# Optimization experiments

Measured on AMD Instinct MI355X. Metric: run time of the kernel, lower is better.

## Reference

```python
import jax, jax.numpy as jnp
import numpy as np

H_IMG = 256; W_IMG = 256; C = 256
WIN = (16, 16); STRIPE = (32, 32); DF = 4; NH = 4
ASZ = (STRIPE[0] // DF, STRIPE[1] // DF)
TS = ((STRIPE[0] + ASZ[0]) // 2, (STRIPE[1] + ASZ[1]) // 2)  # stripe bias table half-size (20,20)


def _win_part(x, ws):
    # (B,H,W,c) -> (B*nW, ws0*ws1, c)
    B, H, W, c = x.shape
    x = x.reshape(B, H // ws[0], ws[0], W // ws[1], ws[1], c)
    return x.transpose(0, 1, 3, 2, 4, 5).reshape(-1, ws[0] * ws[1], c)


def _win_rev(w, ws, H, W):
    c = w.shape[-1]
    B = w.shape[0] // ((H // ws[0]) * (W // ws[1]))
    x = w.reshape(B, H // ws[0], W // ws[1], ws[0], ws[1], c)
    return x.transpose(0, 1, 3, 2, 4, 5).reshape(B, H, W, c)


def _l2n(x):
    # F.normalize(dim=-1)
    return x / jnp.maximum(jnp.linalg.norm(x, axis=-1, keepdims=True), 1e-12)


def _affine(attn, logit_scale, w1, b1, w2, table, index):
    # attn: (B_, nH, N1, N2); AffineTransform with mask=None
    N1, N2 = attn.shape[-2], attn.shape[-1]
    attn = attn * jnp.exp(jnp.minimum(logit_scale, np.log(100.0)))  # clamp max=log(1/0.01)
    bt = jax.nn.relu(table.reshape(-1, 2) @ w1 + b1) @ w2  # (T, nH)
    bias = bt[index.reshape(-1)].reshape(N1, N2, -1).transpose(2, 0, 1)  # (nH,N1,N2)
    return attn + (16.0 * jax.nn.sigmoid(bias))[None]


def _coords(start, size):
    h = np.arange(start[0], start[0] + size[0])
    w = np.arange(start[1], start[1] + size[1])
    return np.stack(np.meshgrid(h, w, indexing='ij')).reshape(2, -1)


def _idx(c1, c2, md):
    d = (c1[:, :, None] - c2[:, None, :]).transpose(1, 2, 0).astype(np.int64)
    return (d[..., 0] + md[0] - 1) * (2 * md[1] - 1) + (d[..., 1] + md[1] - 1)


def _table(ts):
    h = np.arange(-(ts[0] - 1), ts[0], dtype=np.float32) / (ts[0] - 1)
    w = np.arange(-(ts[1] - 1), ts[1], dtype=np.float32) / (ts[1] - 1)
    t = np.stack(np.meshgrid(h, w, indexing='ij'), axis=-1)[None] * 8.0
    return (np.sign(t) * np.log2(np.abs(t) + 1.0) / np.log2(8.0)).astype(np.float32)


def setup_inputs():
    ks = iter(jax.random.split(jax.random.key(0), 32))
    def nrm(shape, s=0.02):
        return jax.random.normal(next(ks), shape, dtype=jnp.float32) * s
    inp = {}
    inp['x'] = jax.random.normal(next(ks), (1, H_IMG * W_IMG, C), dtype=jnp.float32)
    inp['qkv_w'] = nrm((C, 3 * C)); inp['qkv_b'] = nrm((3 * C,))
    inp['anchor_w'] = nrm((C, C // 2)); inp['anchor_b'] = nrm((C // 2,))
    for tag in ['w', 's1', 's2']:
        inp['ls_' + tag] = jnp.full((NH, 1, 1), np.log(10.0), dtype=jnp.float32)
        inp['cpb_w1_' + tag] = nrm((2, 512), 0.1)
        inp['cpb_b1_' + tag] = nrm((512,), 0.1)
        inp['cpb_w2_' + tag] = nrm((512, NH), 0.1)
    inp['proj_w'] = nrm((C, C)); inp['proj_b'] = nrm((C,))
    inp['table_w'] = jnp.asarray(_table(WIN))
    inp['table_s'] = jnp.asarray(_table(TS))
    cw = _coords((0, 0), WIN)
    inp['index_w'] = jnp.asarray(_idx(cw, cw, WIN), dtype=jnp.int32)
    cs = _coords((0, 0), STRIPE)
    st = ((STRIPE[0] - ASZ[0]) // 2, (STRIPE[1] - ASZ[1]) // 2)
    ca = _coords(st, ASZ)
    inp['index_a2w'] = jnp.asarray(_idx(ca, cs, TS), dtype=jnp.int32)
    inp['index_w2a'] = jnp.asarray(_idx(cs, ca, TS), dtype=jnp.int32)
    return inp


def reference(x, qkv_w, qkv_b, anchor_w, anchor_b,
              ls_w, cpb_w1_w, cpb_b1_w, cpb_w2_w,
              ls_s1, cpb_w1_s1, cpb_b1_s1, cpb_w2_s1,
              ls_s2, cpb_w1_s2, cpb_b1_s2, cpb_w2_s2,
              proj_w, proj_b, table_w, table_s,
              index_w, index_a2w, index_w2a):
    B, L, c = x.shape
    qkv = x @ qkv_w + qkv_b               # (B, L, 3C)
    half = 3 * c // 2
    hd = half // 3 // NH                  # head_dim per branch
    # ---- window attention on first half of qkv channels ----
    qw = _win_part(qkv[..., :half].reshape(B, H_IMG, W_IMG, half), WIN)  # (B_, N, 3*C/2)
    B_, N, _ = qw.shape
    q, k, v = qw.reshape(B_, N, 3, NH, hd).transpose(2, 0, 3, 1, 4)
    attn = jnp.einsum('bhnd,bhmd->bhnm', _l2n(q), _l2n(k))
    attn = jax.nn.softmax(_affine(attn, ls_w, cpb_w1_w, cpb_b1_w, cpb_w2_w, table_w, index_w), axis=-1)
    xw = jnp.einsum('bhnm,bhmd->bhnd', attn, v).transpose(0, 2, 1, 3).reshape(B_, N, NH * hd)
    xw = _win_rev(xw, WIN, H_IMG, W_IMG).reshape(B, L, c // 2)
    # ---- anchor projection: AvgPool2d(DF) + Linear(C -> C/2) ----
    xi = x.reshape(B, H_IMG, W_IMG, c)
    pooled = xi.reshape(B, H_IMG // DF, DF, W_IMG // DF, DF, c).mean(axis=(2, 4))
    anchor = pooled @ anchor_w + anchor_b  # (B, H/DF, W/DF, C/2)
    # ---- anchor stripe attention on second half ----
    qs = _win_part(qkv[..., half:].reshape(B, H_IMG, W_IMG, half), STRIPE)  # (Bs, N1, 3*C/2)
    Bs, N1, _ = qs.shape
    anc = _win_part(anchor, ASZ)           # (Bs, N2, C/2)
    N2 = anc.shape[1]
    q, k, v = qs.reshape(Bs, N1, 3, NH, hd).transpose(2, 0, 3, 1, 4)
    anc = anc.reshape(Bs, N2, NH, hd).transpose(0, 2, 1, 3)
    a1 = jnp.einsum('bhnd,bhmd->bhnm', _l2n(anc), _l2n(k))   # (Bs,NH,N2,N1)
    a1 = jax.nn.softmax(_affine(a1, ls_s1, cpb_w1_s1, cpb_b1_s1, cpb_w2_s1, table_s, index_a2w), axis=-1)
    xm = jnp.einsum('bhnm,bhmd->bhnd', a1, v)                # (Bs,NH,N2,hd)
    a2 = jnp.einsum('bhnd,bhmd->bhnm', _l2n(q), _l2n(anc))   # (Bs,NH,N1,N2)
    a2 = jax.nn.softmax(_affine(a2, ls_s2, cpb_w1_s2, cpb_b1_s2, cpb_w2_s2, table_s, index_w2a), axis=-1)
    xs = jnp.einsum('bhnm,bhmd->bhnd', a2, xm).transpose(0, 2, 1, 3).reshape(Bs, N1, NH * hd)
    xs = _win_rev(xs, STRIPE, H_IMG, W_IMG).reshape(B, L, c // 2)
    # ---- merge + output projection ----
    return jnp.concatenate([xw, xs], axis=-1) @ proj_w + proj_b
```

## Files before the change

### kernel.cpp

```cpp
#include <hip/hip_runtime.h>
#include <cstdint>
#include <cstddef>

typedef unsigned short u16;
typedef __attribute__((ext_vector_type(8))) short short8;
typedef __attribute__((ext_vector_type(4))) float floatx4;
typedef __attribute__((ext_vector_type(4))) unsigned int uintx4;
typedef __attribute__((ext_vector_type(2))) unsigned int uintx2;

__device__ __forceinline__ float bf2f(u16 u){
  union { unsigned int i; float f; } v; v.i = ((unsigned int)u) << 16; return v.f;
}
__device__ __forceinline__ u16 f2bf(float f){
  union { float ff; unsigned int i; } v; v.ff = f;
  return (u16)((v.i + 0x7fffu + ((v.i >> 16) & 1u)) >> 16);
}
__device__ __forceinline__ unsigned int pk2(float a, float b){
  return (unsigned int)f2bf(a) | ((unsigned int)f2bf(b) << 16);
}
__device__ __forceinline__ void load32(const u16* p, float* v){
  const uintx4* p4 = (const uintx4*)p;
#pragma unroll
  for (int c = 0; c < 4; ++c){
    uintx4 u = p4[c];
    v[c*8+0] = bf2f((u16)(u.x & 0xffffu)); v[c*8+1] = bf2f((u16)(u.x >> 16));
    v[c*8+2] = bf2f((u16)(u.y & 0xffffu)); v[c*8+3] = bf2f((u16)(u.y >> 16));
    v[c*8+4] = bf2f((u16)(u.z & 0xffffu)); v[c*8+5] = bf2f((u16)(u.z >> 16));
    v[c*8+6] = bf2f((u16)(u.w & 0xffffu)); v[c*8+7] = bf2f((u16)(u.w >> 16));
  }
}
__device__ __forceinline__ void norm_store(u16* dst, const float* v, int t, int strideU16){
  float ss = 0.f;
#pragma unroll
  for (int e = 0; e < 32; ++e) ss += v[e]*v[e];
  float inv = 1.f / fmaxf(sqrtf(ss), 1e-12f);
#pragma unroll
  for (int q = 0; q < 4; ++q){
    uintx4 u;
    u.x = pk2(v[q*8+0]*inv, v[q*8+1]*inv);
    u.y = pk2(v[q*8+2]*inv, v[q*8+3]*inv);
    u.z = pk2(v[q*8+4]*inv, v[q*8+5]*inv);
    u.w = pk2(v[q*8+6]*inv, v[q*8+7]*inv);
    *(uintx4*)(dst + q*strideU16 + t*8) = u;
  }
}
__device__ __forceinline__ float expc(float a){
  return __expf(fminf(a, 30.f));
}
__device__ __forceinline__ uintx4 ld8f_bf(const float* g){
  floatx4 u0 = *(const floatx4*)g;
  floatx4 u1 = *(const floatx4*)(g + 4);
  uintx4 w;
  w.x = pk2(u0.x, u0.y); w.y = pk2(u0.z, u0.w);
  w.z = pk2(u1.x, u1.y); w.w = pk2(u1.z, u1.w);
  return w;
}
__device__ __forceinline__ float redq(float v){
  v += __shfl_xor(v, 16); v += __shfl_xor(v, 32);
  return v;
}

__global__ void transpose_w(const float* __restrict__ qkv_w, const float* __restrict__ anchor_w,
                            const float* __restrict__ proj_w,
                            u16* __restrict__ qkvt, u16* __restrict__ anct, u16* __restrict__ projt){
  int id = blockIdx.x*256 + threadIdx.x;
  if (id < 196608){ int k = id / 768, n = id % 768; qkvt[n*256 + k] = f2bf(qkv_w[id]); }
  else if (id < 229376){ int r = id - 196608; int k = r / 128, n = r % 128; anct[n*256 + k] = f2bf(anchor_w[r]); }
  else { int r = id - 229376; int k = r >> 8, n = r & 255; projt[n*256 + k] = f2bf(proj_w[r]); }
}

__global__ void cpb_mlp(const float* __restrict__ tw, const float* __restrict__ ts,
                        const float* __restrict__ w1w, const float* __restrict__ b1w, const float* __restrict__ w2w,
                        const float* __restrict__ w1s1, const float* __restrict__ b1s1, const float* __restrict__ w2s1,
                        const float* __restrict__ w1s2, const float* __restrict__ b1s2, const float* __restrict__ w2s2,
                        float* __restrict__ btw, float* __restrict__ bts1, float* __restrict__ bts2){
  int tag = blockIdx.y;
  const float *tab, *w1, *b1, *w2; float* bt; int T;
  if (tag == 0){ tab = tw; w1 = w1w;  b1 = b1w;  w2 = w2w;  bt = btw;  T = 961; }
  else if (tag == 1){ tab = ts; w1 = w1s1; b1 = b1s1; w2 = w2s1; bt = bts1; T = 1521; }
  else { tab = ts; w1 = w1s2; b1 = b1s2; w2 = w2s2; bt = bts2; T = 1521; }
  __shared__ float sw1[2][512];
  __shared__ float sb1[512];
  __shared__ float sw2[512][4];
  for (int j = threadIdx.x; j < 512; j += 256){
    sw1[0][j] = w1[j]; sw1[1][j] = w1[512 + j]; sb1[j] = b1[j];
    for (int h = 0; h < 4; ++h) sw2[j][h] = w2[j*4 + h];
  }
  __syncthreads();
  int idx = blockIdx.x*256 + threadIdx.x;
  int r = idx >> 2, hh = idx & 3;
  if (r < T){
    float t0 = tab[2*r], t1 = tab[2*r + 1];
    float acc = 0.f;
    for (int j = 0; j < 512; ++j){
      float hj = fmaxf(fmaf(t0, sw1[0][j], fmaf(t1, sw1[1][j], sb1[j])), 0.f);
      acc = fmaf(hj, sw2[j][hh], acc);
    }
    bt[r*4 + hh] = acc;
  }
}

__global__ void bias_gather(const float* __restrict__ btw, const float* __restrict__ bts1,
                            const float* __restrict__ bts2,
                            const int* __restrict__ idxw, const int* __restrict__ idxa2w,
                            const int* __restrict__ idxw2a,
                            float* __restrict__ bw, float* __restrict__ bs1, float* __restrict__ bs2){
  int id = blockIdx.x*256 + threadIdx.x;
  int which = id >> 18;
  int rem = id & 262143;
  int h = rem >> 16, e = rem & 65535;
  const float* bt; const int* ix; float* dst;
  if (which == 0){ bt = btw;  ix = idxw;   dst = bw;  }
  else if (which == 1){ bt = bts1; ix = idxa2w; dst = bs1; }
  else { bt = bts2; ix = idxw2a; dst = bs2; }
  float v = bt[ix[e]*4 + h];
  dst[h*65536 + e] = 16.f / (1.f + expc(-v));
}

__global__ void avgpool(const float* __restrict__ x, float* __restrict__ pooled){
  int a = blockIdx.x, c = threadIdx.x;
  int ay = a >> 6, ax = a & 63;
  float acc = 0.f;
#pragma unroll
  for (int dy = 0; dy < 4; ++dy)
#pragma unroll
    for (int dx = 0; dx < 4; ++dx)
      acc += x[(size_t)((ay*4 + dy)*256 + ax*4 + dx)*256 + c];
  pooled[(size_t)a*256 + c] = acc * 0.0625f;
}

__launch_bounds__(256, 2)
__global__ void gemm_bt(const float* __restrict__ A, const u16* __restrict__ Bt,
                        const float* __restrict__ bias, u16* __restrict__ C,
                        int M, int N, int K){
  __shared__ __align__(16) u16 lsA[4096];
  __shared__ __align__(16) u16 lsB[4096];
  const int tid = threadIdx.x, lane = tid & 63, wv = tid >> 6;
  const int lane15 = lane & 15, quad = lane >> 4;
  const int wr = wv >> 1, wc = wv & 1;
  const int m0 = blockIdx.x * 128, n0 = blockIdx.y * 128;
  floatx4 acc[4][4] = {};
  for (int k0 = 0; k0 < K; k0 += 32){
    uintx4 ra[2], rb[2];
#pragma unroll
    for (int c = 0; c < 2; ++c){
      int f = c*256 + tid, row = f & 127, q = f >> 7;
      ra[c] = ld8f_bf(A + (size_t)(m0 + row)*K + k0 + q*8);
      rb[c] = *(const uintx4*)(Bt + (size_t)(n0 + row)*K + k0 + q*8);
    }
#pragma unroll
    for (int c = 0; c < 2; ++c){
      int f = c*256 + tid;
      *(uintx4*)(lsA + f*8) = ra[c];
      *(uintx4*)(lsB + f*8) = rb[c];
    }
    __syncthreads();
    short8 a[4], b[4];
#pragma unroll
    for (int i = 0; i < 4; ++i)
      a[i] = *(const short8*)(lsA + quad*1024 + (wr*64 + i*16 + lane15)*8);
#pragma unroll
    for (int j = 0; j < 4; ++j)
      b[j] = *(const short8*)(lsB + quad*1024 + (wc*64 + j*16 + lane15)*8);
#pragma unroll
    for (int i = 0; i < 4; ++i)
#pragma unroll
      for (int j = 0; j < 4; ++j)
        acc[i][j] = __builtin_amdgcn_mfma_f32_16x16x32_bf16(a[i], b[j], acc[i][j], 0, 0, 0);
    __syncthreads();
  }
#pragma unroll
  for (int j = 0; j < 4; ++j){
    int col = n0 + wc*64 + j*16 + lane15;
    float bz = bias[col];
#pragma unroll
    for (int i = 0; i < 4; ++i){
      int rowb = m0 + wr*64 + i*16 + quad*4;
#pragma unroll
      for (int r = 0; r < 4; ++r)
        C[(size_t)(rowb + r)*N + col] = f2bf(acc[i][j][r] + bz);
    }
  }
}

__launch_bounds__(256, 2)
__global__ void gemm_proj_inplace(float* __restrict__ AC, const u16* __restrict__ Bt,
                                  const float* __restrict__ bias){
  __shared__ __align__(16) u16 lsA[4096];
  __shared__ __align__(16) u16 lsB[8192];
  const int tid = threadIdx.x, lane = tid & 63, wv = tid >> 6;
  const int lane15 = lane & 15, quad = lane >> 4;
  const int wr = wv >> 1, wc = wv & 1;
  const int m0 = blockIdx.x * 128;
  floatx4 acc[4][8] = {};
  for (int k0 = 0; k0 < 256; k0 += 32){
    uintx4 ra[2], rb[4];
#pragma unroll
    for (int c = 0; c < 2; ++c){
      int f = c*256 + tid, row = f & 127, q = f >> 7;
      ra[c] = ld8f_bf(AC + (size_t)(m0 + row)*256 + k0 + q*8);
    }
#pragma unroll
    for (int c = 0; c < 4; ++c){
      int f = c*256 + tid, row = f & 255, q = f >> 8;
      rb[c] = *(const uintx4*)(Bt + (size_t)row*256 + k0 + q*8);
    }
#pragma unroll
    for (int c = 0; c < 2; ++c){ int f = c*256 + tid; *(uintx4*)(lsA + f*8) = ra[c]; }
#pragma unroll
    for (int c = 0; c < 4; ++c){ int f = c*256 + tid; *(uintx4*)(lsB + f*8) = rb[c]; }
    __syncthreads();
    short8 a[4], b[8];
#pragma unroll
    for (int i = 0; i < 4; ++i)
      a[i] = *(const short8*)(lsA + quad*1024 + (wr*64 + i*16 + lane15)*8);
#pragma unroll
    for (int j = 0; j < 8; ++j)
      b[j] = *(const short8*)(lsB + quad*2048 + (wc*128 + j*16 + lane15)*8);
#pragma unroll
    for (int i = 0; i < 4; ++i)
#pragma unroll
      for (int j = 0; j < 8; ++j)
        acc[i][j] = __builtin_amdgcn_mfma_f32_16x16x32_bf16(a[i], b[j], acc[i][j], 0, 0, 0);
    __syncthreads();
  }
#pragma unroll
  for (int j = 0; j < 8; ++j){
    int col = wc*128 + j*16 + lane15;
    float bz = bias[col];
#pragma unroll
    for (int i = 0; i < 4; ++i){
      int rowb = m0 + wr*64 + i*16 + quad*4;
#pragma unroll
      for (int r = 0; r < 4; ++r)
        AC[(size_t)(rowb + r)*256 + col] = acc[i][j][r] + bz;
    }
  }
}

__launch_bounds__(256, 3)
__global__ void win_attn(const u16* __restrict__ qkvh, const float* __restrict__ lsw,
                         const float* __restrict__ biasw, float* __restrict__ outm, int r0){
  __shared__ __align__(16) u16 sm[24576];
  const int tid = threadIdx.x, lane = tid & 63, wv = tid >> 6;
  const int lane15 = lane & 15, quad = lane >> 4;
  const int h = blockIdx.y;
  const int wyl = blockIdx.x >> 4, wx = blockIdx.x & 15;
  u16* Ks = sm;
  u16* Qs = sm + 8192;
  u16* VT = sm + 16384;
  {
    int t = tid;
    int pyl = wyl*16 + (t >> 4), px = wx*16 + (t & 15);
    const u16* base = qkvh + (size_t)(pyl*256 + px)*384 + h*32;
    float v[32];
    load32(base, v);        norm_store(Qs, v, t, 2048);
    load32(base + 128, v);  norm_store(Ks, v, t, 2048);
    load32(base + 256, v);
    int kq = t >> 3, e = t & 7;
#pragma unroll
    for (int d = 0; d < 32; ++d) VT[kq*256 + d*8 + e] = f2bf(v[d]);
  }
  __syncthreads();
  short8 qf[4];
#pragma unroll
  for (int j = 0; j < 4; ++j)
    qf[j] = *(const short8*)(Qs + quad*2048 + (wv*64 + j*16 + lane15)*8);
  __syncthreads();

  float scale = __expf(fminf(lsw[h], 4.6051702f));
  float off = fminf(scale + 16.f, 80.f);
  const float* bptr = biasw + ((size_t)h << 16);
  u16* Pw = Qs + wv*2048;
  const floatx4 zf4 = {0.f, 0.f, 0.f, 0.f};
  floatx4 accO[2][4] = {};
  float lsum[4] = {};

  for (int kc = 0; kc < 8; ++kc){
    floatx4 bia[2][4];
#pragma unroll
    for (int i = 0; i < 2; ++i)
#pragma unroll
      for (int j = 0; j < 4; ++j)
        bia[i][j] = *(const floatx4*)(bptr + (size_t)(wv*64 + j*16 + lane15)*256 + kc*32 + i*16 + quad*4);
    short8 kf[2];
#pragma unroll
    for (int i = 0; i < 2; ++i)
      kf[i] = *(const short8*)(Ks + quad*2048 + (kc*32 + i*16 + lane15)*8);
#pragma unroll
    for (int i = 0; i < 2; ++i)
#pragma unroll
      for (int j = 0; j < 4; ++j){
        floatx4 sv = __builtin_amdgcn_mfma_f32_16x16x32_bf16(kf[i], qf[j], zf4, 0, 0, 0);
        float p0 = expc(fmaf(sv[0], scale, bia[i][j][0]) - off);
        float p1 = expc(fmaf(sv[1], scale, bia[i][j][1]) - off);
        float p2 = expc(fmaf(sv[2], scale, bia[i][j][2]) - off);
        float p3 = expc(fmaf(sv[3], scale, bia[i][j][3]) - off);
        lsum[j] += (p0 + p1) + (p2 + p3);
        uintx2 w; w.x = pk2(p0, p1); w.y = pk2(p2, p3);
        *(uintx2*)(Pw + (i*2 + (quad>>1))*512 + (j*16 + lane15)*8 + (quad&1)*4) = w;
      }
    asm volatile("s_waitcnt lgkmcnt(0)" ::: "memory");
    short8 ptf[4], vtf[2];
#pragma unroll
    for (int j = 0; j < 4; ++j)
      ptf[j] = *(const short8*)(Pw + quad*512 + (j*16 + lane15)*8);
#pragma unroll
    for (int m = 0; m < 2; ++m)
      vtf[m] = *(const short8*)(VT + (kc*4 + quad)*256 + (m*16 + lane15)*8);
#pragma unroll
    for (int m = 0; m < 2; ++m)
#pragma unroll
      for (int j = 0; j < 4; ++j)
        accO[m][j] = __builtin_amdgcn_mfma_f32_16x16x32_bf16(vtf[m], ptf[j], accO[m][j], 0, 0, 0);
  }
  float linv[4];
#pragma unroll
  for (int j = 0; j < 4; ++j) linv[j] = 1.f / redq(lsum[j]);
#pragma unroll
  for (int m = 0; m < 2; ++m)
#pragma unroll
    for (int j = 0; j < 4; ++j){
      int tok = wv*64 + j*16 + lane15;
      int py = r0 + wyl*16 + (tok >> 4), px = wx*16 + (tok & 15);
      floatx4 o = accO[m][j] * linv[j];
      *(floatx4*)(outm + (size_t)(py*256 + px)*256 + h*32 + m*16 + quad*4) = o;
    }
}

__launch_bounds__(256, 3)
__global__ void stripe_xm(const u16* __restrict__ qkvh, const u16* __restrict__ anchor,
                          const float* __restrict__ ls1, const float* __restrict__ bias1,
                          float* __restrict__ gl1, u16* __restrict__ gO, int r0){
  __shared__ __align__(16) u16 sm[18432];
  const int tid = threadIdx.x, lane = tid & 63, wv = tid >> 6;
  const int lane15 = lane & 15, quad = lane >> 4;
  const int s = blockIdx.x, h = blockIdx.y, kb = blockIdx.z;
  const int syl = s >> 3, sx = s & 7;
  u16* ANC = sm; u16* KC = sm + 2048; u16* VT = sm + 6144; u16* P1T = sm + 10240;
  if (tid < 64){
    int ay = (r0 >> 2) + syl*8 + (tid >> 3), ax = sx*8 + (tid & 7);
    float v[32]; load32(anchor + (size_t)(ay*64 + ax)*128 + h*32, v);
    norm_store(ANC, v, tid, 512);
  }
  __syncthreads();
  short8 ancf = *(const short8*)(ANC + quad*512 + (wv*16 + lane15)*8);
  float scale1 = __expf(fminf(ls1[h], 4.6051702f));
  float off1 = fminf(scale1 + 16.f, 80.f);
  const float* b1p = bias1 + ((size_t)h << 16) + (size_t)(wv*16 + lane15)*1024;
  const floatx4 zf4 = {0.f, 0.f, 0.f, 0.f};
  floatx4 accO1[2] = {};
  float l1 = 0.f;
  for (int kc = 0; kc < 4; ++kc){
    int kkb = kb*512 + kc*128;
    { int t = tid;
      if (t < 128){
        int tok = kkb + t;
        int pyl = syl*32 + (tok >> 5), px = sx*32 + (tok & 31);
        float v[32]; load32(qkvh + (size_t)(pyl*256 + px)*384 + 128 + h*32, v);
        norm_store(KC, v, t, 1024);
      } else {
        int t2 = t - 128, tok = kkb + t2;
        int pyl = syl*32 + (tok >> 5), px = sx*32 + (tok & 31);
        float v[32]; load32(qkvh + (size_t)(pyl*256 + px)*384 + 256 + h*32, v);
        int kq = t2 >> 3, e = t2 & 7;
#pragma unroll
        for (int d = 0; d < 32; ++d) VT[kq*256 + d*8 + e] = f2bf(v[d]);
      }
    }
    __syncthreads();
    floatx4 bia[8];
#pragma unroll
    for (int i = 0; i < 8; ++i)
      bia[i] = *(const floatx4*)(b1p + kkb + i*16 + quad*4);
#pragma unroll
    for (int i = 0; i < 8; ++i){
      short8 kf = *(const short8*)(KC + quad*1024 + (i*16 + lane15)*8);
      floatx4 sv = __builtin_amdgcn_mfma_f32_16x16x32_bf16(kf, ancf, zf4, 0, 0, 0);
      float p0 = expc(fmaf(sv[0], scale1, bia[i][0]) - off1);
      float p1 = expc(fmaf(sv[1], scale1, bia[i][1]) - off1);
      float p2 = expc(fmaf(sv[2], scale1, bia[i][2]) - off1);
      float p3 = expc(fmaf(sv[3], scale1, bia[i][3]) - off1);
      l1 += (p0 + p1) + (p2 + p3);
      uintx2 w; w.x = pk2(p0, p1); w.y = pk2(p2, p3);
      *(uintx2*)(P1T + (i*2 + (quad>>1))*512 + (wv*16 + lane15)*8 + (quad&1)*4) = w;
    }
    asm volatile("s_waitcnt lgkmcnt(0)" ::: "memory");
#pragma unroll
    for (int ks = 0; ks < 4; ++ks){
      short8 ptf = *(const short8*)(P1T + (ks*4 + quad)*512 + (wv*16 + lane15)*8);
#pragma unroll
      for (int m = 0; m < 2; ++m){
        short8 vtf = *(const short8*)(VT + (ks*4 + quad)*256 + (m*16 + lane15)*8);
        accO1[m] = __builtin_amdgcn_mfma_f32_16x16x32_bf16(vtf, ptf, accO1[m], 0, 0, 0);
      }
    }
    __syncthreads();
  }
  l1 = redq(l1);
  int ent = (s*4 + h)*2 + kb;
  if (quad == 0) gl1[ent*64 + wv*16 + lane15] = l1;
#pragma unroll
  for (int m = 0; m < 2; ++m){
    uintx2 w; w.x = pk2(accO1[m][0], accO1[m][1]); w.y = pk2(accO1[m][2], accO1[m][3]);
    *(uintx2*)(gO + (size_t)ent*2048 + (wv*16 + lane15)*32 + m*16 + quad*4) = w;
  }
}

__launch_bounds__(256, 3)
__global__ void stripe_xs(const u16* __restrict__ qkvh, const u16* __restrict__ anchor,
                          const float* __restrict__ ls2, const float* __restrict__ bias2,
                          const float* __restrict__ gl1, const u16* __restrict__ gO,
                          float* __restrict__ outm, int r0){
  __shared__ __align__(16) u16 sm[20480];
  const int tid = threadIdx.x, lane = tid & 63, wv = tid >> 6;
  const int lane15 = lane & 15, quad = lane >> 4;
  const int s = blockIdx.x >> 2, qc = blockIdx.x & 3, h = blockIdx.y;
  const int syl = s >> 3, sx = s & 7;
  u16* ANC = sm;
  u16* XMT = sm + 2048;
  u16* QW  = sm + 4096 + wv*2048;
  u16* P2T = sm + 12288 + wv*2048;
  if (tid < 64){
    int ay = (r0 >> 2) + syl*8 + (tid >> 3), ax = sx*8 + (tid & 7);
    float v[32]; load32(anchor + (size_t)(ay*64 + ax)*128 + h*32, v);
    norm_store(ANC, v, tid, 512);
  }
  {
    int a = tid >> 2, db = (tid & 3)*8;
    int e0 = (s*4 + h)*2;
    float inv = 1.f / (gl1[e0*64 + a] + gl1[(e0 + 1)*64 + a]);
    uintx4 u0 = *(const uintx4*)(gO + (size_t)e0*2048 + a*32 + db);
    uintx4 u1 = *(const uintx4*)(gO + (size_t)(e0 + 1)*2048 + a*32 + db);
    unsigned int w0[4] = {u0.x, u0.y, u0.z, u0.w};
    unsigned int w1[4] = {u1.x, u1.y, u1.z, u1.w};
#pragma unroll
    for (int c = 0; c < 4; ++c){
      float a0 = bf2f((u16)(w0[c] & 0xffffu)) + bf2f((u16)(w1[c] & 0xffffu));
      float a1 = bf2f((u16)(w0[c] >> 16))     + bf2f((u16)(w1[c] >> 16));
      XMT[(a >> 3)*256 + (db + c*2)*8     + (a & 7)] = f2bf(a0 * inv);
      XMT[(a >> 3)*256 + (db + c*2 + 1)*8 + (a & 7)] = f2bf(a1 * inv);
    }
  }
  __syncthreads();
  int tq = qc*256 + wv*64;
  { int tok = tq + lane;
    int pyl = syl*32 + (tok >> 5), px = sx*32 + (tok & 31);
    float v[32]; load32(qkvh + (size_t)(pyl*256 + px)*384 + h*32, v);
    norm_store(QW, v, lane, 512);
  }
  asm volatile("s_waitcnt lgkmcnt(0)" ::: "memory");
  short8 qf2[4];
#pragma unroll
  for (int j = 0; j < 4; ++j)
    qf2[j] = *(const short8*)(QW + quad*512 + (j*16 + lane15)*8);
  float scale2 = __expf(fminf(ls2[h], 4.6051702f));
  float off2 = fminf(scale2 + 16.f, 80.f);
  const float* b2p = bias2 + ((size_t)h << 16);
  const floatx4 zf4 = {0.f, 0.f, 0.f, 0.f};
  floatx4 accO2[2][4] = {};
  float l2[4] = {};
#pragma unroll
  for (int c = 0; c < 2; ++c){
    floatx4 bia[2][4];
#pragma unroll
    for (int i = 0; i < 2; ++i)
#pragma unroll
      for (int j = 0; j < 4; ++j)
        bia[i][j] = *(const floatx4*)(b2p + (size_t)(tq + j*16 + lane15)*64 + c*32 + i*16 + quad*4);
    short8 af[2];
#pragma unroll
    for (int i = 0; i < 2; ++i)
      af[i] = *(const short8*)(ANC + quad*512 + (c*32 + i*16 + lane15)*8);
#pragma unroll
    for (int i = 0; i < 2; ++i)
#pragma unroll
      for (int j = 0; j < 4; ++j){
        floatx4 sv = __builtin_amdgcn_mfma_f32_16x16x32_bf16(af[i], qf2[j], zf4, 0, 0, 0);
        float p0 = expc(fmaf(sv[0], scale2, bia[i][j][0]) - off2);
        float p1 = expc(fmaf(sv[1], scale2, bia[i][j][1]) - off2);
        float p2 = expc(fmaf(sv[2], scale2, bia[i][j][2]) - off2);
        float p3 = expc(fmaf(sv[3], scale2, bia[i][j][3]) - off2);
        l2[j] += (p0 + p1) + (p2 + p3);
        uintx2 w; w.x = pk2(p0, p1); w.y = pk2(p2, p3);
        *(uintx2*)(P2T + (i*2 + (quad>>1))*512 + (j*16 + lane15)*8 + (quad&1)*4) = w;
      }
    asm volatile("s_waitcnt lgkmcnt(0)" ::: "memory");
    short8 ptf[4], xmf[2];
#pragma unroll
    for (int j = 0; j < 4; ++j)
      ptf[j] = *(const short8*)(P2T + quad*512 + (j*16 + lane15)*8);
#pragma unroll
    for (int m = 0; m < 2; ++m)
      xmf[m] = *(const short8*)(XMT + (c*4 + quad)*256 + (m*16 + lane15)*8);
#pragma unroll
    for (int m = 0; m < 2; ++m)
#pragma unroll
      for (int j = 0; j < 4; ++j)
        accO2[m][j] = __builtin_amdgcn_mfma_f32_16x16x32_bf16(xmf[m], ptf[j], accO2[m][j], 0, 0, 0);
  }
  float linv[4];
#pragma unroll
  for (int j = 0; j < 4; ++j) linv[j] = 1.f / redq(l2[j]);
#pragma unroll
  for (int m = 0; m < 2; ++m)
#pragma unroll
    for (int j = 0; j < 4; ++j){
      int tok = tq + j*16 + lane15;
      int py = r0 + syl*32 + (tok >> 5), px = sx*32 + (tok & 31);
      floatx4 o = accO2[m][j] * linv[j];
      *(floatx4*)(outm + (size_t)(py*256 + px)*256 + 128 + h*32 + m*16 + quad*4) = o;
    }
}

extern "C" void kernel_launch(void* const* d_in, const int* in_sizes, int n_in,
                              void* d_out, int out_size, void* d_ws, size_t ws_size,
                              hipStream_t stream) {
  (void)in_sizes; (void)n_in; (void)out_size; (void)ws_size;
  const float* x        = (const float*)d_in[0];
  const float* qkv_w    = (const float*)d_in[1];
  const float* qkv_b    = (const float*)d_in[2];
  const float* anchor_w = (const float*)d_in[3];
  const float* anchor_b = (const float*)d_in[4];
  const float* ls_w     = (const float*)d_in[5];
  const float* w1_w     = (const float*)d_in[6];
  const float* b1_w     = (const float*)d_in[7];
  const float* w2_w     = (const float*)d_in[8];
  const float* ls_s1    = (const float*)d_in[9];
  const float* w1_s1    = (const float*)d_in[10];
  const float* b1_s1    = (const float*)d_in[11];
  const float* w2_s1    = (const float*)d_in[12];
  const float* ls_s2    = (const float*)d_in[13];
  const float* w1_s2    = (const float*)d_in[14];
  const float* b1_s2    = (const float*)d_in[15];
  const float* w2_s2    = (const float*)d_in[16];
  const float* proj_w   = (const float*)d_in[17];
  const float* proj_b   = (const float*)d_in[18];
  const float* table_w  = (const float*)d_in[19];
  const float* table_s  = (const float*)d_in[20];
  const int* index_w   = (const int*)d_in[21];
  const int* index_a2w = (const int*)d_in[22];
  const int* index_w2a = (const int*)d_in[23];

  char* ws = (char*)d_ws;
  u16*   qkvh   = (u16*)(ws + 0);
  float* pooled = (float*)(ws + 0);
  u16*   anch   = (u16*)(ws + 25165824);
  u16*   qkvt   = (u16*)(ws + 26214400);
  u16*   anct   = (u16*)(ws + 26607616);
  u16*   projt  = (u16*)(ws + 26673152);
  float* btw    = (float*)(ws + 26804224);
  float* bts1   = (float*)(ws + 26820608);
  float* bts2   = (float*)(ws + 26845184);
  float* biasw  = (float*)(ws + 26869760);
  float* bias1  = (float*)(ws + 27918336);
  float* bias2  = (float*)(ws + 28966912);
  float* gl1    = (float*)(ws + 30015488);
  u16*   gO     = (u16*)(ws + 30081024);

  float* merged = (float*)d_out;

  transpose_w<<<1152, 256, 0, stream>>>(qkv_w, anchor_w, proj_w, qkvt, anct, projt);
  cpb_mlp<<<dim3(24, 3), 256, 0, stream>>>(table_w, table_s,
                                           w1_w, b1_w, w2_w,
                                           w1_s1, b1_s1, w2_s1,
                                           w1_s2, b1_s2, w2_s2,
                                           btw, bts1, bts2);
  bias_gather<<<3072, 256, 0, stream>>>(btw, bts1, bts2, index_w, index_a2w, index_w2a,
                                        biasw, bias1, bias2);
  avgpool<<<4096, 256, 0, stream>>>(x, pooled);
  gemm_bt<<<dim3(32, 1), 256, 0, stream>>>(pooled, anct, anchor_b, anch, 4096, 128, 256);

  for (int half = 0; half < 2; ++half){
    const float* xh = x + (size_t)half*32768*256;
    int r0 = half*128;
    gemm_bt<<<dim3(256, 3), 256, 0, stream>>>(xh, qkvt, qkv_b, qkvh, 32768, 384, 256);
    win_attn<<<dim3(128, 4), 256, 0, stream>>>(qkvh, ls_w, biasw, merged, r0);
    gemm_bt<<<dim3(256, 3), 256, 0, stream>>>(xh, qkvt + 384*256, qkv_b + 384, qkvh, 32768, 384, 256);
    stripe_xm<<<dim3(32, 4, 2), 256, 0, stream>>>(qkvh, anch, ls_s1, bias1, gl1, gO, r0);
    stripe_xs<<<dim3(128, 4), 256, 0, stream>>>(qkvh, anch, ls_s2, bias2, gl1, gO, merged, r0);
  }

  gemm_proj_inplace<<<dim3(512), 256, 0, stream>>>(merged, projt, proj_b);
}
```

Measured before the change: 407.4 us.

## Use direct global-to-LDS loads, swizzled LDS, vector stores, and exp2 softmax

The GEMM kernels now stage the bf16 weight tile straight into LDS with global_load_lds and place the A tile in a rotated LDS layout to cut bank conflicts. Swapping the MFMA operand order lets the epilogue write contiguous vectorised bf16 or fp32 stores. The softmax folds the logit scale, offset and log2e into the precomputed bias table so each score costs one fma plus exp2, and bf16 conversion uses the hardware convert intrinsic. This removes the 30.0 exp clamp and changes rounding behaviour slightly.

```diff
diff --git a/kernel.cpp b/kernel.cpp
--- a/kernel.cpp
+++ b/kernel.cpp
@@ -5,18 +5,27 @@
 typedef unsigned short u16;
 typedef __attribute__((ext_vector_type(8))) short short8;
 typedef __attribute__((ext_vector_type(4))) float floatx4;
+typedef __attribute__((ext_vector_type(2))) float floatx2;
 typedef __attribute__((ext_vector_type(4))) unsigned int uintx4;
 typedef __attribute__((ext_vector_type(2))) unsigned int uintx2;
+typedef __attribute__((ext_vector_type(2))) __bf16 bf16x2;
+
+#define LOG2E 1.44269504f
 
 __device__ __forceinline__ float bf2f(u16 u){
   union { unsigned int i; float f; } v; v.i = ((unsigned int)u) << 16; return v.f;
 }
 __device__ __forceinline__ u16 f2bf(float f){
-  union { float ff; unsigned int i; } v; v.ff = f;
-  return (u16)((v.i + 0x7fffu + ((v.i >> 16) & 1u)) >> 16);
+  union { __bf16 b; u16 u; } v; v.b = (__bf16)f; return v.u;
 }
 __device__ __forceinline__ unsigned int pk2(float a, float b){
-  return (unsigned int)f2bf(a) | ((unsigned int)f2bf(b) << 16);
+  union { bf16x2 h; unsigned int u; } v;
+  v.h = __builtin_convertvector((floatx2){a, b}, bf16x2);
+  return v.u;
+}
+__device__ __forceinline__ void gload16(const void* g, void* l){
+  __builtin_amdgcn_global_load_lds((const __attribute__((address_space(1))) unsigned int*)g,
+                                   (__attribute__((address_space(3))) unsigned int*)l, 16, 0, 0);
 }
 __device__ __forceinline__ void load32(const u16* p, float* v){
   const uintx4* p4 = (const uintx4*)p;
@@ -43,9 +52,6 @@
     u.w = pk2(v[q*8+6]*inv, v[q*8+7]*inv);
     *(uintx4*)(dst + q*strideU16 + t*8) = u;
   }
-}
-__device__ __forceinline__ float expc(float a){
-  return __expf(fminf(a, 30.f));
 }
 __device__ __forceinline__ uintx4 ld8f_bf(const float* g){
   floatx4 u0 = *(const floatx4*)g;
@@ -104,17 +110,22 @@
                             const float* __restrict__ bts2,
                             const int* __restrict__ idxw, const int* __restrict__ idxa2w,
                             const int* __restrict__ idxw2a,
+                            const float* __restrict__ lsw, const float* __restrict__ ls1,
+                            const float* __restrict__ ls2,
                             float* __restrict__ bw, float* __restrict__ bs1, float* __restrict__ bs2){
   int id = blockIdx.x*256 + threadIdx.x;
   int which = id >> 18;
   int rem = id & 262143;
   int h = rem >> 16, e = rem & 65535;
-  const float* bt; const int* ix; float* dst;
-  if (which == 0){ bt = btw;  ix = idxw;   dst = bw;  }
-  else if (which == 1){ bt = bts1; ix = idxa2w; dst = bs1; }
-  else { bt = bts2; ix = idxw2a; dst = bs2; }
+  const float* bt; const int* ix; float* dst; const float* ls;
+  if (which == 0){ bt = btw;  ix = idxw;   dst = bw;  ls = lsw; }
+  else if (which == 1){ bt = bts1; ix = idxa2w; dst = bs1; ls = ls1; }
+  else { bt = bts2; ix = idxw2a; dst = bs2; ls = ls2; }
   float v = bt[ix[e]*4 + h];
-  dst[h*65536 + e] = 16.f / (1.f + expc(-v));
+  float scale = exp2f(fminf(ls[h], 4.6051702f) * LOG2E);
+  float off = fminf(scale + 16.f, 80.f);
+  float sig = 16.f / (1.f + exp2f(-v * LOG2E));
+  dst[h*65536 + e] = (sig - off) * LOG2E;
 }
 
 __global__ void avgpool(const float* __restrict__ x, float* __restrict__ pooled){
@@ -133,52 +144,56 @@
 __global__ void gemm_bt(const float* __restrict__ A, const u16* __restrict__ Bt,
                         const float* __restrict__ bias, u16* __restrict__ C,
                         int M, int N, int K){
+  (void)M;
   __shared__ __align__(16) u16 lsA[4096];
   __shared__ __align__(16) u16 lsB[4096];
   const int tid = threadIdx.x, lane = tid & 63, wv = tid >> 6;
   const int lane15 = lane & 15, quad = lane >> 4;
   const int wr = wv >> 1, wc = wv & 1;
   const int m0 = blockIdx.x * 128, n0 = blockIdx.y * 128;
+  char* lsBb = (char*)lsB;
+  const int brow = wv*16 + (lane >> 2);
+  const u16* bsrc = Bt + (size_t)(n0 + brow)*K + (lane & 3)*8;
+  const int arow = tid & 127, aq = tid >> 7;
+  const float* asrc = A + (size_t)(m0 + arow)*K;
+  const int aslot0 = aq*1024 + ((arow + aq*2) & 127)*8;
+  const int aslot1 = (aq+2)*1024 + ((arow + (aq+2)*2) & 127)*8;
   floatx4 acc[4][4] = {};
   for (int k0 = 0; k0 < K; k0 += 32){
-    uintx4 ra[2], rb[2];
-#pragma unroll
-    for (int c = 0; c < 2; ++c){
-      int f = c*256 + tid, row = f & 127, q = f >> 7;
-      ra[c] = ld8f_bf(A + (size_t)(m0 + row)*K + k0 + q*8);
-      rb[c] = *(const uintx4*)(Bt + (size_t)(n0 + row)*K + k0 + q*8);
-    }
-#pragma unroll
-    for (int c = 0; c < 2; ++c){
-      int f = c*256 + tid;
-      *(uintx4*)(lsA + f*8) = ra[c];
-      *(uintx4*)(lsB + f*8) = rb[c];
-    }
+    gload16(bsrc + k0,                 lsBb + wv*1024);
+    gload16(bsrc + (size_t)64*K + k0,  lsBb + 4096 + wv*1024);
+    uintx4 ra0 = ld8f_bf(asrc + k0 + aq*8);
+    uintx4 ra1 = ld8f_bf(asrc + k0 + (aq+2)*8);
+    *(uintx4*)(lsA + aslot0) = ra0;
+    *(uintx4*)(lsA + aslot1) = ra1;
     __syncthreads();
     short8 a[4], b[4];
 #pragma unroll
+    for (int i = 0; i < 4; ++i){
+      int r = wr*64 + i*16 + lane15;
+      a[i] = *(const short8*)(lsA + quad*1024 + ((r + quad*2) & 127)*8);
+    }
+#pragma unroll
+    for (int j = 0; j < 4; ++j)
+      b[j] = *(const short8*)(lsBb + (wc*64 + j*16 + lane15)*64 + quad*16);
+#pragma unroll
     for (int i = 0; i < 4; ++i)
-      a[i] = *(const short8*)(lsA + quad*1024 + (wr*64 + i*16 + lane15)*8);
-#pragma unroll
-    for (int j = 0; j < 4; ++j)
-      b[j] = *(const short8*)(lsB + quad*1024 + (wc*64 + j*16 + lane15)*8);
-#pragma unroll
-    for (int i = 0; i < 4; ++i)
 #pragma unroll
       for (int j = 0; j < 4; ++j)
-        acc[i][j] = __builtin_amdgcn_mfma_f32_16x16x32_bf16(a[i], b[j], acc[i][j], 0, 0, 0);
+        acc[i][j] = __builtin_amdgcn_mfma_f32_16x16x32_bf16(b[j], a[i], acc[i][j], 0, 0, 0);
     __syncthreads();
   }
 #pragma unroll
-  for (int j = 0; j < 4; ++j){
-    int col = n0 + wc*64 + j*16 + lane15;
-    float bz = bias[col];
-#pragma unroll
-    for (int i = 0; i < 4; ++i){
-      int rowb = m0 + wr*64 + i*16 + quad*4;
-#pragma unroll
-      for (int r = 0; r < 4; ++r)
-        C[(size_t)(rowb + r)*N + col] = f2bf(acc[i][j][r] + bz);
+  for (int i = 0; i < 4; ++i){
+    int row = m0 + wr*64 + i*16 + lane15;
+#pragma unroll
+    for (int j = 0; j < 4; ++j){
+      int colb = n0 + wc*64 + j*16 + quad*4;
+      floatx4 bz = *(const floatx4*)(bias + colb);
+      uintx2 w;
+      w.x = pk2(acc[i][j][0] + bz.x, acc[i][j][1] + bz.y);
+      w.y = pk2(acc[i][j][2] + bz.z, acc[i][j][3] + bz.w);
+      *(uintx2*)(C + (size_t)row*N + colb) = w;
     }
   }
 }
@@ -192,48 +207,49 @@
   const int lane15 = lane & 15, quad = lane >> 4;
   const int wr = wv >> 1, wc = wv & 1;
   const int m0 = blockIdx.x * 128;
+  char* lsBb = (char*)lsB;
+  const int brow = wv*16 + (lane >> 2);
+  const u16* bsrc = Bt + (size_t)brow*256 + (lane & 3)*8;
+  const int arow = tid & 127, aq = tid >> 7;
+  const float* asrc = AC + (size_t)(m0 + arow)*256;
+  const int aslot0 = aq*1024 + ((arow + aq*2) & 127)*8;
+  const int aslot1 = (aq+2)*1024 + ((arow + (aq+2)*2) & 127)*8;
   floatx4 acc[4][8] = {};
   for (int k0 = 0; k0 < 256; k0 += 32){
-    uintx4 ra[2], rb[4];
-#pragma unroll
-    for (int c = 0; c < 2; ++c){
-      int f = c*256 + tid, row = f & 127, q = f >> 7;
-      ra[c] = ld8f_bf(AC + (size_t)(m0 + row)*256 + k0 + q*8);
-    }
-#pragma unroll
-    for (int c = 0; c < 4; ++c){
-      int f = c*256 + tid, row = f & 255, q = f >> 8;
-      rb[c] = *(const uintx4*)(Bt + (size_t)row*256 + k0 + q*8);
-    }
-#pragma unroll
-    for (int c = 0; c < 2; ++c){ int f = c*256 + tid; *(uintx4*)(lsA + f*8) = ra[c]; }
-#pragma unroll
-    for (int c = 0; c < 4; ++c){ int f = c*256 + tid; *(uintx4*)(lsB + f*8) = rb[c]; }
+    gload16(bsrc + k0,                lsBb +         wv*1024);
+    gload16(bsrc + 64*256 + k0,       lsBb + 4096  + wv*1024);
+    gload16(bsrc + 128*256 + k0,      lsBb + 8192  + wv*1024);
+    gload16(bsrc + 192*256 + k0,      lsBb + 12288 + wv*1024);
+    uintx4 ra0 = ld8f_bf(asrc + k0 + aq*8);
+    uintx4 ra1 = ld8f_bf(asrc + k0 + (aq+2)*8);
+    *(uintx4*)(lsA + aslot0) = ra0;
+    *(uintx4*)(lsA + aslot1) = ra1;
     __syncthreads();
     short8 a[4], b[8];
 #pragma unroll
+    for (int i = 0; i < 4; ++i){
+      int r = wr*64 + i*16 + lane15;
+      a[i] = *(const short8*)(lsA + quad*1024 + ((r + quad*2) & 127)*8);
+    }
+#pragma unroll
+    for (int j = 0; j < 8; ++j)
+      b[j] = *(const short8*)(lsBb + (wc*128 + j*16 + lane15)*64 + quad*16);
+#pragma unroll
     for (int i = 0; i < 4; ++i)
-      a[i] = *(const short8*)(lsA + quad*1024 + (wr*64 + i*16 + lane15)*8);
-#pragma unroll
-    for (int j = 0; j < 8; ++j)
-      b[j] = *(const short8*)(lsB + quad*2048 + (wc*128 + j*16 + lane15)*8);
-#pragma unroll
-    for (int i = 0; i < 4; ++i)
 #pragma unroll
       for (int j = 0; j < 8; ++j)
-        acc[i][j] = __builtin_amdgcn_mfma_f32_16x16x32_bf16(a[i], b[j], acc[i][j], 0, 0, 0);
+        acc[i][j] = __builtin_amdgcn_mfma_f32_16x16x32_bf16(b[j], a[i], acc[i][j], 0, 0, 0);
     __syncthreads();
   }
 #pragma unroll
-  for (int j = 0; j < 8; ++j){
-    int col = wc*128 + j*16 + lane15;
-    float bz = bias[col];
-#pragma unroll
-    for (int i = 0; i < 4; ++i){
-      int rowb = m0 + wr*64 + i*16 + quad*4;
-#pragma unroll
-      for (int r = 0; r < 4; ++r)
-        AC[(size_t)(rowb + r)*256 + col] = acc[i][j][r] + bz;
+  for (int i = 0; i < 4; ++i){
+    int row = m0 + wr*64 + i*16 + lane15;
+#pragma unroll
+    for (int j = 0; j < 8; ++j){
+      int colb = wc*128 + j*16 + quad*4;
+      floatx4 bz = *(const floatx4*)(bias + colb);
+      floatx4 o = acc[i][j] + bz;
+      *(floatx4*)(AC + (size_t)row*256 + colb) = o;
     }
   }
 }
@@ -268,8 +284,7 @@
     qf[j] = *(const short8*)(Qs + quad*2048 + (wv*64 + j*16 + lane15)*8);
   __syncthreads();
 
-  float scale = __expf(fminf(lsw[h], 4.6051702f));
-  float off = fminf(scale + 16.f, 80.f);
+  float scale = exp2f(fminf(lsw[h], 4.6051702f) * LOG2E) * LOG2E;
   const float* bptr = biasw + ((size_t)h << 16);
   u16* Pw = Qs + wv*2048;
   const floatx4 zf4 = {0.f, 0.f, 0.f, 0.f};
@@ -292,10 +307,10 @@
 #pragma unroll
       for (int j = 0; j < 4; ++j){
         floatx4 sv = __builtin_amdgcn_mfma_f32_16x16x32_bf16(kf[i], qf[j], zf4, 0, 0, 0);
-        float p0 = expc(fmaf(sv[0], scale, bia[i][j][0]) - off);
-        float p1 = expc(fmaf(sv[1], scale, bia[i][j][1]) - off);
-        float p2 = expc(fmaf(sv[2], scale, bia[i][j][2]) - off);
-        float p3 = expc(fmaf(sv[3], scale, bia[i][j][3]) - off);
+        float p0 = exp2f(fmaf(sv[0], scale, bia[i][j][0]));
+        float p1 = exp2f(fmaf(sv[1], scale, bia[i][j][1]));
+        float p2 = exp2f(fmaf(sv[2], scale, bia[i][j][2]));
+        float p3 = exp2f(fmaf(sv[3], scale, bia[i][j][3]));
         lsum[j] += (p0 + p1) + (p2 + p3);
         uintx2 w; w.x = pk2(p0, p1); w.y = pk2(p2, p3);
         *(uintx2*)(Pw + (i*2 + (quad>>1))*512 + (j*16 + lane15)*8 + (quad&1)*4) = w;
@@ -345,8 +360,7 @@
   }
   __syncthreads();
   short8 ancf = *(const short8*)(ANC + quad*512 + (wv*16 + lane15)*8);
-  float scale1 = __expf(fminf(ls1[h], 4.6051702f));
-  float off1 = fminf(scale1 + 16.f, 80.f);
+  float scale1 = exp2f(fminf(ls1[h], 4.6051702f) * LOG2E) * LOG2E;
   const float* b1p = bias1 + ((size_t)h << 16) + (size_t)(wv*16 + lane15)*1024;
   const floatx4 zf4 = {0.f, 0.f, 0.f, 0.f};
   floatx4 accO1[2] = {};
@@ -377,10 +391,10 @@
     for (int i = 0; i < 8; ++i){
       short8 kf = *(const short8*)(KC + quad*1024 + (i*16 + lane15)*8);
       floatx4 sv = __builtin_amdgcn_mfma_f32_16x16x32_bf16(kf, ancf, zf4, 0, 0, 0);
-      float p0 = expc(fmaf(sv[0], scale1, bia[i][0]) - off1);
-      float p1 = expc(fmaf(sv[1], scale1, bia[i][1]) - off1);
-      float p2 = expc(fmaf(sv[2], scale1, bia[i][2]) - off1);
-      float p3 = expc(fmaf(sv[3], scale1, bia[i][3]) - off1);
+      float p0 = exp2f(fmaf(sv[0], scale1, bia[i][0]));
+      float p1 = exp2f(fmaf(sv[1], scale1, bia[i][1]));
+      float p2 = exp2f(fmaf(sv[2], scale1, bia[i][2]));
+      float p3 = exp2f(fmaf(sv[3], scale1, bia[i][3]));
       l1 += (p0 + p1) + (p2 + p3);
       uintx2 w; w.x = pk2(p0, p1); w.y = pk2(p2, p3);
       *(uintx2*)(P1T + (i*2 + (quad>>1))*512 + (wv*16 + lane15)*8 + (quad&1)*4) = w;
@@ -454,8 +468,7 @@
 #pragma unroll
   for (int j = 0; j < 4; ++j)
     qf2[j] = *(const short8*)(QW + quad*512 + (j*16 + lane15)*8);
-  float scale2 = __expf(fminf(ls2[h], 4.6051702f));
-  float off2 = fminf(scale2 + 16.f, 80.f);
+  float scale2 = exp2f(fminf(ls2[h], 4.6051702f) * LOG2E) * LOG2E;
   const float* b2p = bias2 + ((size_t)h << 16);
   const floatx4 zf4 = {0.f, 0.f, 0.f, 0.f};
   floatx4 accO2[2][4] = {};
@@ -477,10 +490,10 @@
 #pragma unroll
       for (int j = 0; j < 4; ++j){
         floatx4 sv = __builtin_amdgcn_mfma_f32_16x16x32_bf16(af[i], qf2[j], zf4, 0, 0, 0);
-        float p0 = expc(fmaf(sv[0], scale2, bia[i][j][0]) - off2);
-        float p1 = expc(fmaf(sv[1], scale2, bia[i][j][1]) - off2);
-        float p2 = expc(fmaf(sv[2], scale2, bia[i][j][2]) - off2);
-        float p3 = expc(fmaf(sv[3], scale2, bia[i][j][3]) - off2);
+        float p0 = exp2f(fmaf(sv[0], scale2, bia[i][j][0]));
+        float p1 = exp2f(fmaf(sv[1], scale2, bia[i][j][1]));
+        float p2 = exp2f(fmaf(sv[2], scale2, bia[i][j][2]));
+        float p3 = exp2f(fmaf(sv[3], scale2, bia[i][j][3]));
         l2[j] += (p0 + p1) + (p2 + p3);
         uintx2 w; w.x = pk2(p0, p1); w.y = pk2(p2, p3);
         *(uintx2*)(P2T + (i*2 + (quad>>1))*512 + (j*16 + lane15)*8 + (quad&1)*4) = w;
@@ -567,7 +580,7 @@
                                            w1_s2, b1_s2, w2_s2,
                                            btw, bts1, bts2);
   bias_gather<<<3072, 256, 0, stream>>>(btw, bts1, bts2, index_w, index_a2w, index_w2a,
-                                        biasw, bias1, bias2);
+                                        ls_w, ls_s1, ls_s2, biasw, bias1, bias2);
   avgpool<<<4096, 256, 0, stream>>>(x, pooled);
   gemm_bt<<<dim3(32, 1), 256, 0, stream>>>(pooled, anct, anchor_b, anch, 4096, 128, 256);
 
```

Result: no change. 399.6 us (-1.9%).
